# Kernel optimization log

Hardware: AMD Instinct MI355X
Metric: run time of the kernel (lower is better)

## Reference

```python
import jax, jax.numpy as jnp
import numpy as np

D_MODEL = 1024
NUM_HEADS = 16
D_K = D_MODEL // NUM_HEADS
B, S = 2, 2048


def setup_inputs() -> dict:
    key = jax.random.key(0)
    ks = jax.random.split(key, 11)
    lim = 1.0 / np.sqrt(D_MODEL)  # torch Linear default init range
    def lin(kw, kb):
        W = jax.random.uniform(kw, (D_MODEL, D_MODEL), jnp.float32, -lim, lim)
        b = jax.random.uniform(kb, (D_MODEL,), jnp.float32, -lim, lim)
        return W, b
    Wq, bq = lin(ks[0], ks[1])
    Wk, bk = lin(ks[2], ks[3])
    Wv, bv = lin(ks[4], ks[5])
    Wo, bo = lin(ks[6], ks[7])
    return {
        "Q": jax.random.normal(ks[8], (B, S, D_MODEL), jnp.float32),
        "K": jax.random.normal(ks[9], (B, S, D_MODEL), jnp.float32),
        "V": jax.random.normal(ks[10], (B, S, D_MODEL), jnp.float32),
        "Wq": Wq, "bq": bq, "Wk": Wk, "bk": bk,
        "Wv": Wv, "bv": bv, "Wo": Wo, "bo": bo,
        "validate": False,
    }


def _split_heads(x):
    b, s, _ = x.shape
    return x.reshape(b, s, NUM_HEADS, D_K).transpose(0, 2, 1, 3)  # [B,H,S,Dk]


def reference(Q, K, V, Wq, bq, Wk, bk, Wv, bv, Wo, bo, validate):
    # Linear projections (torch Linear: x @ W.T + b)
    q = _split_heads(Q @ Wq.T + bq)
    k = _split_heads(K @ Wk.T + bk)
    v = _split_heads(V @ Wv.T + bv)
    scale = 1.0 / jnp.sqrt(jnp.asarray(D_K, q.dtype))
    scores = jnp.einsum("bhqd,bhkd->bhqk", q, k) * scale  # [B,H,S,S]
    attn = jax.nn.softmax(scores, axis=-1)
    out = jnp.einsum("bhqk,bhkd->bhqd", attn, v)  # [B,H,S,Dk]
    out = out.transpose(0, 2, 1, 3).reshape(Q.shape[0], Q.shape[1], D_MODEL)
    return out @ Wo.T + bo
```

## Files before the change

kernel.cpp:

```cpp
#include <hip/hip_runtime.h>


typedef short bf16x8 __attribute__((ext_vector_type(8)));
typedef float f32x4 __attribute__((ext_vector_type(4)));

#define D_MODEL 1024
#define NHEAD 16
#define DK 64
#define BB 2
#define SS 2048
#define MROWS (BB * SS)
#define C1 0.18033688011112042f

__device__ __forceinline__ unsigned short f2bf(float f) {
  unsigned u = __builtin_bit_cast(unsigned, f);
  u += 0x7fffu + ((u >> 16) & 1u);
  return (unsigned short)(u >> 16);
}
__device__ __forceinline__ unsigned pack2(float a, float b) {
  return (unsigned)f2bf(a) | ((unsigned)f2bf(b) << 16);
}
__device__ __forceinline__ unsigned cvtpk(float lo, float hi) {
  unsigned r;
  asm("v_cvt_pk_bf16_f32 %0, %1, %2" : "=v"(r) : "v"(lo), "v"(hi));
  return r;
}
__device__ __forceinline__ float max3f(float a, float b, float c) {
  float d;
  asm("v_max3_f32 %0, %1, %2, %3" : "=v"(d) : "v"(a), "v"(b), "v"(c));
  return d;
}

typedef __attribute__((address_space(3))) unsigned int as3u;
typedef const __attribute__((address_space(1))) unsigned int as1u;
__device__ __forceinline__ void gload16(void* lds, const void* g) {
  __builtin_amdgcn_global_load_lds((as1u*)g, (as3u*)lds, 16, 0, 0);
}

struct CvtArgs {
  const float* s[7];
  unsigned short* d[7];
  int n8[7];
};

__global__ __launch_bounds__(256) void convert_bf16(CvtArgs a) {
  const int slot = blockIdx.y;
  const float* __restrict__ s = a.s[slot];
  unsigned short* __restrict__ d = a.d[slot];
  const int n8 = a.n8[slot];
  for (int i = blockIdx.x * 256 + threadIdx.x; i < n8; i += gridDim.x * 256) {
    const size_t off = (size_t)i * 8;
    const float4 v0 = *(const float4*)&s[off];
    const float4 v1 = *(const float4*)&s[off + 4];
    uint4 p;
    p.x = pack2(v0.x, v0.y); p.y = pack2(v0.z, v0.w);
    p.z = pack2(v1.x, v1.y); p.w = pack2(v1.z, v1.w);
    *(uint4*)&d[off] = p;
  }
}

template <int BM, int BN, int MODE>
__device__ __forceinline__ void gemm_core(unsigned short* smem,
                                          const unsigned short* __restrict__ A,
                                          const unsigned short* __restrict__ B,
                                          const float* __restrict__ bias,
                                          float scale, float* __restrict__ Cf,
                                          unsigned short* __restrict__ Cb) {
  const int LDSZ = (BM + BN) * 64;
  const int tid = threadIdx.x;
  const int lane = tid & 63, w = tid >> 6;
  const int wm = w >> 1, wn = w & 1;
  const int l15 = lane & 15, l4 = lane >> 4;
  const int bm = blockIdx.y, bn = blockIdx.x;
  const int MF = BM / 32, NF = BN / 32;

  auto stage = [&](unsigned short* dst, int k0) {
    unsigned short* Asb = dst;
    unsigned short* Bsb = dst + BM * 64;
#pragma unroll
    for (int i = 0; i < BM / 32; ++i) {
      const int flat = i * 256 + tid;
      const int row = flat >> 3, g = flat & 7;
      gload16(&Asb[flat * 8], &A[(size_t)(bm * BM + row) * D_MODEL + k0 + ((g ^ (row & 7)) << 3)]);
    }
#pragma unroll
    for (int i = 0; i < BN / 32; ++i) {
      const int flat = i * 256 + tid;
      const int row = flat >> 3, g = flat & 7;
      gload16(&Bsb[flat * 8], &B[(size_t)(bn * BN + row) * D_MODEL + k0 + ((g ^ (row & 7)) << 3)]);
    }
  };

  f32x4 acc[MF][NF];
#pragma unroll
  for (int m = 0; m < MF; ++m)
#pragma unroll
    for (int n = 0; n < NF; ++n) acc[m][n] = (f32x4){0.f, 0.f, 0.f, 0.f};

  stage(smem, 0);
  __syncthreads();
  int cur = 0;
  for (int k0 = 0; k0 < D_MODEL; k0 += 64) {
    if (k0 + 64 < D_MODEL) stage(smem + (cur ^ 1) * LDSZ, k0 + 64);
    unsigned short* As = smem + cur * LDSZ;
    unsigned short* Bs = As + BM * 64;
#pragma unroll
    for (int kk = 0; kk < 2; ++kk) {
      bf16x8 af[MF], bf[NF];
#pragma unroll
      for (int m = 0; m < MF; ++m) {
        const int r = wm * (BM / 2) + m * 16 + l15;
        af[m] = *(const bf16x8*)&As[r * 64 + (((kk * 4 + l4) ^ (r & 7)) << 3)];
      }
#pragma unroll
      for (int n = 0; n < NF; ++n) {
        const int r = wn * (BN / 2) + n * 16 + l15;
        bf[n] = *(const bf16x8*)&Bs[r * 64 + (((kk * 4 + l4) ^ (r & 7)) << 3)];
      }
#pragma unroll
      for (int m = 0; m < MF; ++m)
#pragma unroll
        for (int n = 0; n < NF; ++n)
          acc[m][n] = __builtin_amdgcn_mfma_f32_16x16x32_bf16(af[m], bf[n], acc[m][n], 0, 0, 0);
    }
    __syncthreads();
    cur ^= 1;
  }

  if (MODE != 2) {
#pragma unroll
    for (int m = 0; m < MF; ++m)
#pragma unroll
      for (int n = 0; n < NF; ++n) {
        const int col = bn * BN + wn * (BN / 2) + n * 16 + l15;
        const float bv = bias[col];
#pragma unroll
        for (int r = 0; r < 4; ++r) {
          const int row = bm * BM + wm * (BM / 2) + m * 16 + l4 * 4 + r;
          const float v = (acc[m][n][r] + bv) * scale;
          if (MODE == 0) Cb[(size_t)row * D_MODEL + col] = f2bf(v);
          else           Cf[(size_t)row * D_MODEL + col] = v;
        }
      }
  } else {
    unsigned short* T = smem;
#pragma unroll
    for (int m = 0; m < MF; ++m)
#pragma unroll
      for (int n = 0; n < NF; ++n) {
        const int cl = wn * (BN / 2) + n * 16 + l15;
        const float bv = bias[bn * BN + cl];
#pragma unroll
        for (int r = 0; r < 4; ++r) {
          const int rl = wm * (BM / 2) + m * 16 + l4 * 4 + r;
          const int byte = cl * (BM * 2) + ((((rl >> 3) ^ (cl & 7))) << 4) + ((rl & 7) << 1);
          *(unsigned short*)((char*)T + byte) = f2bf(acc[m][n][r] + bv);
        }
      }
    __syncthreads();
#pragma unroll
    for (int c = 0; c < BN * BM / 8 / 256; ++c) {
      const int chunk = c * 256 + tid;
      const int cl = chunk >> 3, rl0 = (chunk & 7) * 8;
      const int byte = cl * (BM * 2) + (((rl0 >> 3) ^ (cl & 7)) << 4);
      const uint4 val = *(const uint4*)((const char*)T + byte);
      const int gcol = bn * BN + cl;
      const int bb = (bm * BM) >> 11;
      const int s = ((bm * BM) & 2047) + rl0;
      *(uint4*)&Cb[(size_t)(bb * 1024 + gcol) * SS + s] = val;
    }
  }
}

__global__ __launch_bounds__(256, 3) void gemm_qkv(
    const unsigned short* __restrict__ Xq, const unsigned short* __restrict__ Xk,
    const unsigned short* __restrict__ Xv,
    const unsigned short* __restrict__ Wq, const float* __restrict__ bq,
    const unsigned short* __restrict__ Wk, const float* __restrict__ bk,
    const unsigned short* __restrict__ Wv, const float* __restrict__ bv,
    unsigned short* __restrict__ q, unsigned short* __restrict__ k,
    unsigned short* __restrict__ vT) {
  __shared__ __align__(16) unsigned short smem[2 * (64 + 128) * 64];
  const int z = blockIdx.z;
  if (z == 0) {
    gemm_core<64, 128, 0>(smem, Xq, Wq, bq, C1, nullptr, q);
  } else if (z == 1) {
    gemm_core<64, 128, 0>(smem, Xk, Wk, bk, 1.0f, nullptr, k);
  } else {
    gemm_core<64, 128, 2>(smem, Xv, Wv, bv, 1.0f, nullptr, vT);
  }
}

__global__ __launch_bounds__(256, 3) void gemm_o(const unsigned short* __restrict__ A,
                                                 const unsigned short* __restrict__ W,
                                                 const float* __restrict__ bi,
                                                 float* __restrict__ out) {
  __shared__ __align__(16) unsigned short smem[2 * (64 + 128) * 64];
  gemm_core<64, 128, 1>(smem, A, W, bi, 1.0f, out, nullptr);
}

__global__ __launch_bounds__(256, 4) void attn_kernel(
    const unsigned short* __restrict__ Qp, const unsigned short* __restrict__ Kp,
    const unsigned short* __restrict__ vTp, unsigned short* __restrict__ Op) {
  __shared__ __align__(16) unsigned short Kt[2][64 * 64];
  __shared__ __align__(16) unsigned short Vt[2][64 * 64];
  __shared__ __align__(16) unsigned short Pt[4][16 * 64];
  const int tid = threadIdx.x;
  const int lane = tid & 63, w = tid >> 6;
  const int l15 = lane & 15, l4 = lane >> 4;
  const int bh = blockIdx.x;
  const int b = bh >> 4, h = bh & 15;
  const int qb = blockIdx.y;
  const size_t baseQ = (size_t)b * SS * D_MODEL + (size_t)h * DK;
  const size_t baseV = (size_t)(b * 1024 + h * 64) * SS;

  const int qrow = qb * 64 + w * 16 + l15;
  bf16x8 aq[2];
#pragma unroll
  for (int kk = 0; kk < 2; ++kk)
    aq[kk] = *(const bf16x8*)&Qp[baseQ + (size_t)qrow * D_MODEL + kk * 32 + l4 * 8];

  const bf16x8 vone = {0x3F80, 0x3F80, 0x3F80, 0x3F80, 0x3F80, 0x3F80, 0x3F80, 0x3F80};

  float rm = -1e30f;
  f32x4 acc[5];
#pragma unroll
  for (int d = 0; d < 5; ++d) acc[d] = (f32x4){0.f, 0.f, 0.f, 0.f};

  auto stage = [&](int buf, int kt) {
#pragma unroll
    for (int i = 0; i < 2; ++i) {
      const int flat = (w * 2 + i) * 64 + lane;
      const int row = flat >> 3, g = flat & 7;
      gload16(&Kt[buf][flat * 8],
              &Kp[baseQ + (size_t)(kt * 64 + row) * D_MODEL + ((g ^ (row & 7)) << 3)]);
    }
#pragma unroll
    for (int i = 0; i < 2; ++i) {
      const int flat = (w * 2 + i) * 64 + lane;
      const int row = flat >> 3, g = flat & 7;
      gload16(&Vt[buf][flat * 8],
              &vTp[baseV + (size_t)row * SS + kt * 64 + ((g ^ (row & 7)) << 3)]);
    }
  };

  stage(0, 0);
  __syncthreads();
  int cur = 0;
  for (int kt = 0; kt < SS / 64; ++kt) {
    if (kt + 1 < SS / 64) stage(cur ^ 1, kt + 1);

    f32x4 st[4];
#pragma unroll
    for (int n = 0; n < 4; ++n) st[n] = (f32x4){0.f, 0.f, 0.f, 0.f};
#pragma unroll
    for (int kk = 0; kk < 2; ++kk) {
      bf16x8 kf[4];
#pragma unroll
      for (int n = 0; n < 4; ++n) {
        const int r = n * 16 + l15;
        kf[n] = *(const bf16x8*)&Kt[cur][r * 64 + (((kk * 4 + l4) ^ (r & 7)) << 3)];
      }
#pragma unroll
      for (int n = 0; n < 4; ++n)
        st[n] = __builtin_amdgcn_mfma_f32_16x16x32_bf16(kf[n], aq[kk], st[n], 0, 0, 0);
    }

    const float a0 = max3f(st[0][0], st[0][1], st[0][2]);
    const float a1 = max3f(st[0][3], st[1][0], st[1][1]);
    const float a2 = max3f(st[1][2], st[1][3], st[2][0]);
    const float a3 = max3f(st[2][1], st[2][2], st[2][3]);
    const float a4 = max3f(st[3][0], st[3][1], st[3][2]);
    float mx = fmaxf(max3f(a0, a1, a2), max3f(a3, a4, st[3][3]));
    mx = fmaxf(mx, __shfl_xor(mx, 16));
    mx = fmaxf(mx, __shfl_xor(mx, 32));
    if (__any(mx > rm + 8.f)) {
      const float nm = fmaxf(rm, mx);
      const float alpha = exp2f(rm - nm);
      rm = nm;
#pragma unroll
      for (int r = 0; r < 4; ++r) {
        const float ar = __shfl(alpha, l4 * 4 + r);
#pragma unroll
        for (int d = 0; d < 5; ++d) acc[d][r] *= ar;
      }
    }
#pragma unroll
    for (int n = 0; n < 4; ++n)
#pragma unroll
      for (int r = 0; r < 4; ++r) st[n][r] = exp2f(st[n][r] - rm);

#pragma unroll
    for (int n = 0; n < 4; ++n)
#pragma unroll
      for (int c = 0; c < 2; ++c) {
        const int col = n * 16 + l4 * 4 + 2 * c;
        const int sw = (((col >> 3) ^ (l15 & 7)) << 3) + (col & 7);
        *(unsigned*)&Pt[w][l15 * 64 + sw] = cvtpk(st[n][2 * c], st[n][2 * c + 1]);
      }

#pragma unroll
    for (int kk = 0; kk < 2; ++kk) {
      const bf16x8 ap = *(const bf16x8*)&Pt[w][l15 * 64 + (((kk * 4 + l4) ^ (l15 & 7)) << 3)];
      bf16x8 vf[4];
#pragma unroll
      for (int d = 0; d < 4; ++d) {
        const int r = d * 16 + l15;
        vf[d] = *(const bf16x8*)&Vt[cur][r * 64 + (((kk * 4 + l4) ^ (r & 7)) << 3)];
      }
#pragma unroll
      for (int d = 0; d < 4; ++d)
        acc[d] = __builtin_amdgcn_mfma_f32_16x16x32_bf16(ap, vf[d], acc[d], 0, 0, 0);
      acc[4] = __builtin_amdgcn_mfma_f32_16x16x32_bf16(ap, vone, acc[4], 0, 0, 0);
    }

    __syncthreads();
    cur ^= 1;
  }

  float inv[4];
#pragma unroll
  for (int r = 0; r < 4; ++r) inv[r] = 1.0f / acc[4][r];
#pragma unroll
  for (int d = 0; d < 4; ++d)
#pragma unroll
    for (int r = 0; r < 4; ++r) {
      const int orow = qb * 64 + w * 16 + l4 * 4 + r;
      Op[baseQ + (size_t)orow * D_MODEL + d * 16 + l15] = f2bf(acc[d][r] * inv[r]);
    }
}

extern "C" void kernel_launch(void* const* d_in, const int* in_sizes, int n_in,
                              void* d_out, int out_size, void* d_ws, size_t ws_size,
                              hipStream_t stream) {
  const float* Qin = (const float*)d_in[0];
  const float* Kin = (const float*)d_in[1];
  const float* Vin = (const float*)d_in[2];
  const float* Wq = (const float*)d_in[3];
  const float* bq = (const float*)d_in[4];
  const float* Wk = (const float*)d_in[5];
  const float* bk = (const float*)d_in[6];
  const float* Wv = (const float*)d_in[7];
  const float* bv = (const float*)d_in[8];
  const float* Wo = (const float*)d_in[9];
  const float* bo = (const float*)d_in[10];
  float* out = (float*)d_out;

  const size_t NX = (size_t)MROWS * D_MODEL;
  const size_t NW = (size_t)D_MODEL * D_MODEL;
  unsigned short* ws = (unsigned short*)d_ws;
  unsigned short* q  = ws;
  unsigned short* k  = ws + NX;
  unsigned short* vT = ws + 2 * NX;
  unsigned short* Xq = ws + 3 * NX;
  unsigned short* Xk = ws + 4 * NX;
  unsigned short* Xv = ws + 5 * NX;
  unsigned short* wq = ws + 6 * NX;
  unsigned short* wk = wq + NW;
  unsigned short* wv = wk + NW;
  unsigned short* wo = wv + NW;
  unsigned short* ao = Xq;

  CvtArgs ca;
  ca.s[0] = Qin; ca.d[0] = Xq; ca.n8[0] = (int)(NX / 8);
  ca.s[1] = Kin; ca.d[1] = Xk; ca.n8[1] = (int)(NX / 8);
  ca.s[2] = Vin; ca.d[2] = Xv; ca.n8[2] = (int)(NX / 8);
  ca.s[3] = Wq;  ca.d[3] = wq; ca.n8[3] = (int)(NW / 8);
  ca.s[4] = Wk;  ca.d[4] = wk; ca.n8[4] = (int)(NW / 8);
  ca.s[5] = Wv;  ca.d[5] = wv; ca.n8[5] = (int)(NW / 8);
  ca.s[6] = Wo;  ca.d[6] = wo; ca.n8[6] = (int)(NW / 8);
  convert_bf16<<<dim3(1024, 7), 256, 0, stream>>>(ca);

  gemm_qkv<<<dim3(D_MODEL / 128, MROWS / 64, 3), 256, 0, stream>>>(
      Xq, Xk, Xv, wq, bq, wk, bk, wv, bv, q, k, vT);
  attn_kernel<<<dim3(BB * NHEAD, SS / 64), 256, 0, stream>>>(q, k, vT, ao);
  gemm_o<<<dim3(D_MODEL / 128, MROWS / 64), 256, 0, stream>>>(ao, wo, bo, out);
}
```

Measured before the change: 237.2 us.

## Halve GEMM K-tile, shrink output GEMM tile, double attention query rows per warp

The shared GEMM core now stages 32-wide K slices instead of 64, using a new XOR swizzle. This halves LDS use and allows more resident blocks, at the cost of twice as many loop iterations and barriers. The output projection uses 64x64 tiles, giving twice as many blocks. The attention kernel processes 32 query rows per warp (128 per block) so each K/V tile staged in LDS is reused across two MFMA row groups, with launch bounds lowered to account for the higher register pressure.

Result: slower. 252.8 us (+6.6%).

```diff
diff --git a/kernel.cpp b/kernel.cpp
--- a/kernel.cpp
+++ b/kernel.cpp
@@ -66,7 +66,7 @@
                                           const float* __restrict__ bias,
                                           float scale, float* __restrict__ Cf,
                                           unsigned short* __restrict__ Cb) {
-  const int LDSZ = (BM + BN) * 64;
+  const int LDSZ = (BM + BN) * 32;
   const int tid = threadIdx.x;
   const int lane = tid & 63, w = tid >> 6;
   const int wm = w >> 1, wn = w & 1;
@@ -76,18 +76,20 @@
 
   auto stage = [&](unsigned short* dst, int k0) {
     unsigned short* Asb = dst;
-    unsigned short* Bsb = dst + BM * 64;
-#pragma unroll
-    for (int i = 0; i < BM / 32; ++i) {
+    unsigned short* Bsb = dst + BM * 32;
+#pragma unroll
+    for (int i = 0; i < BM / 64; ++i) {
       const int flat = i * 256 + tid;
-      const int row = flat >> 3, g = flat & 7;
-      gload16(&Asb[flat * 8], &A[(size_t)(bm * BM + row) * D_MODEL + k0 + ((g ^ (row & 7)) << 3)]);
-    }
-#pragma unroll
-    for (int i = 0; i < BN / 32; ++i) {
+      const int row = flat >> 2, gl = flat & 3;
+      const int gs = (gl ^ ((row >> 1) & 3)) * 8;
+      gload16(&Asb[flat * 8], &A[(size_t)(bm * BM + row) * D_MODEL + k0 + gs]);
+    }
+#pragma unroll
+    for (int i = 0; i < BN / 64; ++i) {
       const int flat = i * 256 + tid;
-      const int row = flat >> 3, g = flat & 7;
-      gload16(&Bsb[flat * 8], &B[(size_t)(bn * BN + row) * D_MODEL + k0 + ((g ^ (row & 7)) << 3)]);
+      const int row = flat >> 2, gl = flat & 3;
+      const int gs = (gl ^ ((row >> 1) & 3)) * 8;
+      gload16(&Bsb[flat * 8], &B[(size_t)(bn * BN + row) * D_MODEL + k0 + gs]);
     }
   };
 
@@ -100,29 +102,26 @@
   stage(smem, 0);
   __syncthreads();
   int cur = 0;
-  for (int k0 = 0; k0 < D_MODEL; k0 += 64) {
-    if (k0 + 64 < D_MODEL) stage(smem + (cur ^ 1) * LDSZ, k0 + 64);
+  for (int k0 = 0; k0 < D_MODEL; k0 += 32) {
+    if (k0 + 32 < D_MODEL) stage(smem + (cur ^ 1) * LDSZ, k0 + 32);
     unsigned short* As = smem + cur * LDSZ;
-    unsigned short* Bs = As + BM * 64;
-#pragma unroll
-    for (int kk = 0; kk < 2; ++kk) {
-      bf16x8 af[MF], bf[NF];
-#pragma unroll
-      for (int m = 0; m < MF; ++m) {
-        const int r = wm * (BM / 2) + m * 16 + l15;
-        af[m] = *(const bf16x8*)&As[r * 64 + (((kk * 4 + l4) ^ (r & 7)) << 3)];
-      }
-#pragma unroll
-      for (int n = 0; n < NF; ++n) {
-        const int r = wn * (BN / 2) + n * 16 + l15;
-        bf[n] = *(const bf16x8*)&Bs[r * 64 + (((kk * 4 + l4) ^ (r & 7)) << 3)];
-      }
-#pragma unroll
-      for (int m = 0; m < MF; ++m)
-#pragma unroll
-        for (int n = 0; n < NF; ++n)
-          acc[m][n] = __builtin_amdgcn_mfma_f32_16x16x32_bf16(af[m], bf[n], acc[m][n], 0, 0, 0);
-    }
+    unsigned short* Bs = As + BM * 32;
+    bf16x8 af[MF], bf[NF];
+#pragma unroll
+    for (int m = 0; m < MF; ++m) {
+      const int r = wm * (BM / 2) + m * 16 + l15;
+      af[m] = *(const bf16x8*)&As[r * 32 + ((((r >> 1) & 3) ^ l4) << 3)];
+    }
+#pragma unroll
+    for (int n = 0; n < NF; ++n) {
+      const int r = wn * (BN / 2) + n * 16 + l15;
+      bf[n] = *(const bf16x8*)&Bs[r * 32 + ((((r >> 1) & 3) ^ l4) << 3)];
+    }
+#pragma unroll
+    for (int m = 0; m < MF; ++m)
+#pragma unroll
+      for (int n = 0; n < NF; ++n)
+        acc[m][n] = __builtin_amdgcn_mfma_f32_16x16x32_bf16(af[m], bf[n], acc[m][n], 0, 0, 0);
     __syncthreads();
     cur ^= 1;
   }
@@ -172,7 +171,7 @@
   }
 }
 
-__global__ __launch_bounds__(256, 3) void gemm_qkv(
+__global__ __launch_bounds__(256, 6) void gemm_qkv(
     const unsigned short* __restrict__ Xq, const unsigned short* __restrict__ Xk,
     const unsigned short* __restrict__ Xv,
     const unsigned short* __restrict__ Wq, const float* __restrict__ bq,
@@ -180,7 +179,7 @@
     const unsigned short* __restrict__ Wv, const float* __restrict__ bv,
     unsigned short* __restrict__ q, unsigned short* __restrict__ k,
     unsigned short* __restrict__ vT) {
-  __shared__ __align__(16) unsigned short smem[2 * (64 + 128) * 64];
+  __shared__ __align__(16) unsigned short smem[2 * (64 + 128) * 32];
   const int z = blockIdx.z;
   if (z == 0) {
     gemm_core<64, 128, 0>(smem, Xq, Wq, bq, C1, nullptr, q);
@@ -191,20 +190,20 @@
   }
 }
 
-__global__ __launch_bounds__(256, 3) void gemm_o(const unsigned short* __restrict__ A,
+__global__ __launch_bounds__(256, 4) void gemm_o(const unsigned short* __restrict__ A,
                                                  const unsigned short* __restrict__ W,
                                                  const float* __restrict__ bi,
                                                  float* __restrict__ out) {
-  __shared__ __align__(16) unsigned short smem[2 * (64 + 128) * 64];
-  gemm_core<64, 128, 1>(smem, A, W, bi, 1.0f, out, nullptr);
-}
-
-__global__ __launch_bounds__(256, 4) void attn_kernel(
+  __shared__ __align__(16) unsigned short smem[2 * (64 + 64) * 32];
+  gemm_core<64, 64, 1>(smem, A, W, bi, 1.0f, out, nullptr);
+}
+
+__global__ __launch_bounds__(256, 2) void attn_kernel(
     const unsigned short* __restrict__ Qp, const unsigned short* __restrict__ Kp,
     const unsigned short* __restrict__ vTp, unsigned short* __restrict__ Op) {
   __shared__ __align__(16) unsigned short Kt[2][64 * 64];
   __shared__ __align__(16) unsigned short Vt[2][64 * 64];
-  __shared__ __align__(16) unsigned short Pt[4][16 * 64];
+  __shared__ __align__(16) unsigned short Pt[4][32 * 64];
   const int tid = threadIdx.x;
   const int lane = tid & 63, w = tid >> 6;
   const int l15 = lane & 15, l4 = lane >> 4;
@@ -214,18 +213,23 @@
   const size_t baseQ = (size_t)b * SS * D_MODEL + (size_t)h * DK;
   const size_t baseV = (size_t)(b * 1024 + h * 64) * SS;
 
-  const int qrow = qb * 64 + w * 16 + l15;
-  bf16x8 aq[2];
-#pragma unroll
-  for (int kk = 0; kk < 2; ++kk)
-    aq[kk] = *(const bf16x8*)&Qp[baseQ + (size_t)qrow * D_MODEL + kk * 32 + l4 * 8];
+  bf16x8 aq[2][2];
+#pragma unroll
+  for (int m = 0; m < 2; ++m) {
+    const int qrow = qb * 128 + w * 32 + m * 16 + l15;
+#pragma unroll
+    for (int kk = 0; kk < 2; ++kk)
+      aq[m][kk] = *(const bf16x8*)&Qp[baseQ + (size_t)qrow * D_MODEL + kk * 32 + l4 * 8];
+  }
 
   const bf16x8 vone = {0x3F80, 0x3F80, 0x3F80, 0x3F80, 0x3F80, 0x3F80, 0x3F80, 0x3F80};
 
-  float rm = -1e30f;
-  f32x4 acc[5];
-#pragma unroll
-  for (int d = 0; d < 5; ++d) acc[d] = (f32x4){0.f, 0.f, 0.f, 0.f};
+  float rm[2] = {-1e30f, -1e30f};
+  f32x4 acc[2][5];
+#pragma unroll
+  for (int m = 0; m < 2; ++m)
+#pragma unroll
+    for (int d = 0; d < 5; ++d) acc[m][d] = (f32x4){0.f, 0.f, 0.f, 0.f};
 
   auto stage = [&](int buf, int kt) {
 #pragma unroll
@@ -250,9 +254,11 @@
   for (int kt = 0; kt < SS / 64; ++kt) {
     if (kt + 1 < SS / 64) stage(cur ^ 1, kt + 1);
 
-    f32x4 st[4];
-#pragma unroll
-    for (int n = 0; n < 4; ++n) st[n] = (f32x4){0.f, 0.f, 0.f, 0.f};
+    f32x4 st[2][4];
+#pragma unroll
+    for (int m = 0; m < 2; ++m)
+#pragma unroll
+      for (int n = 0; n < 4; ++n) st[m][n] = (f32x4){0.f, 0.f, 0.f, 0.f};
 #pragma unroll
     for (int kk = 0; kk < 2; ++kk) {
       bf16x8 kf[4];
@@ -262,72 +268,97 @@
         kf[n] = *(const bf16x8*)&Kt[cur][r * 64 + (((kk * 4 + l4) ^ (r & 7)) << 3)];
       }
 #pragma unroll
+      for (int m = 0; m < 2; ++m)
+#pragma unroll
+        for (int n = 0; n < 4; ++n)
+          st[m][n] = __builtin_amdgcn_mfma_f32_16x16x32_bf16(kf[n], aq[m][kk], st[m][n], 0, 0, 0);
+    }
+
+    float mx[2];
+#pragma unroll
+    for (int m = 0; m < 2; ++m) {
+      const float a0 = max3f(st[m][0][0], st[m][0][1], st[m][0][2]);
+      const float a1 = max3f(st[m][0][3], st[m][1][0], st[m][1][1]);
+      const float a2 = max3f(st[m][1][2], st[m][1][3], st[m][2][0]);
+      const float a3 = max3f(st[m][2][1], st[m][2][2], st[m][2][3]);
+      const float a4 = max3f(st[m][3][0], st[m][3][1], st[m][3][2]);
+      float v = fmaxf(max3f(a0, a1, a2), max3f(a3, a4, st[m][3][3]));
+      v = fmaxf(v, __shfl_xor(v, 16));
+      v = fmaxf(v, __shfl_xor(v, 32));
+      mx[m] = v;
+    }
+    if (__any((mx[0] > rm[0] + 8.f) | (mx[1] > rm[1] + 8.f))) {
+#pragma unroll
+      for (int m = 0; m < 2; ++m) {
+        const float nm = fmaxf(rm[m], mx[m]);
+        const float alpha = exp2f(rm[m] - nm);
+        rm[m] = nm;
+#pragma unroll
+        for (int r = 0; r < 4; ++r) {
+          const float ar = __shfl(alpha, l4 * 4 + r);
+#pragma unroll
+          for (int d = 0; d < 5; ++d) acc[m][d][r] *= ar;
+        }
+      }
+    }
+#pragma unroll
+    for (int m = 0; m < 2; ++m)
+#pragma unroll
       for (int n = 0; n < 4; ++n)
-        st[n] = __builtin_amdgcn_mfma_f32_16x16x32_bf16(kf[n], aq[kk], st[n], 0, 0, 0);
-    }
-
-    const float a0 = max3f(st[0][0], st[0][1], st[0][2]);
-    const float a1 = max3f(st[0][3], st[1][0], st[1][1]);
-    const float a2 = max3f(st[1][2], st[1][3], st[2][0]);
-    const float a3 = max3f(st[2][1], st[2][2], st[2][3]);
-    const float a4 = max3f(st[3][0], st[3][1], st[3][2]);
-    float mx = fmaxf(max3f(a0, a1, a2), max3f(a3, a4, st[3][3]));
-    mx = fmaxf(mx, __shfl_xor(mx, 16));
-    mx = fmaxf(mx, __shfl_xor(mx, 32));
-    if (__any(mx > rm + 8.f)) {
-      const float nm = fmaxf(rm, mx);
-      const float alpha = exp2f(rm - nm);
-      rm = nm;
-#pragma unroll
-      for (int r = 0; r < 4; ++r) {
-        const float ar = __shfl(alpha, l4 * 4 + r);
-#pragma unroll
-        for (int d = 0; d < 5; ++d) acc[d][r] *= ar;
-      }
-    }
-#pragma unroll
-    for (int n = 0; n < 4; ++n)
-#pragma unroll
-      for (int r = 0; r < 4; ++r) st[n][r] = exp2f(st[n][r] - rm);
-
-#pragma unroll
-    for (int n = 0; n < 4; ++n)
-#pragma unroll
-      for (int c = 0; c < 2; ++c) {
-        const int col = n * 16 + l4 * 4 + 2 * c;
-        const int sw = (((col >> 3) ^ (l15 & 7)) << 3) + (col & 7);
-        *(unsigned*)&Pt[w][l15 * 64 + sw] = cvtpk(st[n][2 * c], st[n][2 * c + 1]);
-      }
+#pragma unroll
+        for (int r = 0; r < 4; ++r) st[m][n][r] = exp2f(st[m][n][r] - rm[m]);
+
+#pragma unroll
+    for (int m = 0; m < 2; ++m)
+#pragma unroll
+      for (int n = 0; n < 4; ++n)
+#pragma unroll
+        for (int c = 0; c < 2; ++c) {
+          const int col = n * 16 + l4 * 4 + 2 * c;
+          const int row = m * 16 + l15;
+          const int sw = (((col >> 3) ^ (row & 7)) << 3) + (col & 7);
+          *(unsigned*)&Pt[w][row * 64 + sw] = cvtpk(st[m][n][2 * c], st[m][n][2 * c + 1]);
+        }
 
 #pragma unroll
     for (int kk = 0; kk < 2; ++kk) {
-      const bf16x8 ap = *(const bf16x8*)&Pt[w][l15 * 64 + (((kk * 4 + l4) ^ (l15 & 7)) << 3)];
-      bf16x8 vf[4];
+      bf16x8 ap[2], vf[4];
+#pragma unroll
+      for (int m = 0; m < 2; ++m) {
+        const int r = m * 16 + l15;
+        ap[m] = *(const bf16x8*)&Pt[w][r * 64 + (((kk * 4 + l4) ^ (r & 7)) << 3)];
+      }
 #pragma unroll
       for (int d = 0; d < 4; ++d) {
         const int r = d * 16 + l15;
         vf[d] = *(const bf16x8*)&Vt[cur][r * 64 + (((kk * 4 + l4) ^ (r & 7)) << 3)];
       }
 #pragma unroll
-      for (int d = 0; d < 4; ++d)
-        acc[d] = __builtin_amdgcn_mfma_f32_16x16x32_bf16(ap, vf[d], acc[d], 0, 0, 0);
-      acc[4] = __builtin_amdgcn_mfma_f32_16x16x32_bf16(ap, vone, acc[4], 0, 0, 0);
+      for (int m = 0; m < 2; ++m) {
+#pragma unroll
+        for (int d = 0; d < 4; ++d)
+          acc[m][d] = __builtin_amdgcn_mfma_f32_16x16x32_bf16(ap[m], vf[d], acc[m][d], 0, 0, 0);
+        acc[m][4] = __builtin_amdgcn_mfma_f32_16x16x32_bf16(ap[m], vone, acc[m][4], 0, 0, 0);
+      }
     }
 
     __syncthreads();
     cur ^= 1;
   }
 
-  float inv[4];
-#pragma unroll
-  for (int r = 0; r < 4; ++r) inv[r] = 1.0f / acc[4][r];
-#pragma unroll
-  for (int d = 0; d < 4; ++d)
-#pragma unroll
-    for (int r = 0; r < 4; ++r) {
-      const int orow = qb * 64 + w * 16 + l4 * 4 + r;
-      Op[baseQ + (size_t)orow * D_MODEL + d * 16 + l15] = f2bf(acc[d][r] * inv[r]);
-    }
+#pragma unroll
+  for (int m = 0; m < 2; ++m) {
+    float inv[4];
+#pragma unroll
+    for (int r = 0; r < 4; ++r) inv[r] = 1.0f / acc[m][4][r];
+#pragma unroll
+    for (int d = 0; d < 4; ++d)
+#pragma unroll
+      for (int r = 0; r < 4; ++r) {
+        const int orow = qb * 128 + w * 32 + m * 16 + l4 * 4 + r;
+        Op[baseQ + (size_t)orow * D_MODEL + d * 16 + l15] = f2bf(acc[m][d][r] * inv[r]);
+      }
+  }
 }
 
 extern "C" void kernel_launch(void* const* d_in, const int* in_sizes, int n_in,
@@ -373,6 +404,6 @@
 
   gemm_qkv<<<dim3(D_MODEL / 128, MROWS / 64, 3), 256, 0, stream>>>(
       Xq, Xk, Xv, wq, bq, wk, bk, wv, bv, q, k, vT);
-  attn_kernel<<<dim3(BB * NHEAD, SS / 64), 256, 0, stream>>>(q, k, vT, ao);
-  gemm_o<<<dim3(D_MODEL / 128, MROWS / 64), 256, 0, stream>>>(ao, wo, bo, out);
-}
+  attn_kernel<<<dim3(BB * NHEAD, SS / 128), 256, 0, stream>>>(q, k, vT, ao);
+  gemm_o<<<dim3(D_MODEL / 64, MROWS / 64), 256, 0, stream>>>(ao, wo, bo, out);
+}
```
